# Optimization experiments

Measured on AMD Instinct MI355X. Metric: run time of the kernel, lower is better.

## Reference

```python
import jax, jax.numpy as jnp
import numpy as np

N_NODES = 100000
D = 256
N_TYPES = 4
E1 = 300000
E2 = 300000


def setup_inputs() -> dict:
    key = jax.random.key(0)
    ks = jax.random.split(key, 9)
    x = jax.random.normal(ks[0], (N_NODES, D), dtype=jnp.float32)
    hyperedge_index_s1 = jax.random.randint(ks[1], (2, E1 * 1), 0, N_NODES, dtype=jnp.int32)
    hyperedge_type_s1 = jax.random.randint(ks[2], (E1,), 0, N_TYPES, dtype=jnp.int32)
    hyperedge_index_s2 = jax.random.randint(ks[3], (2, E2 * 2), 0, N_NODES, dtype=jnp.int32)
    hyperedge_type_s2 = jax.random.randint(ks[4], (E2,), 0, N_TYPES, dtype=jnp.int32)
    # xavier_normal init for A: std = sqrt(2 / (fan_in + fan_out))
    A_s1 = jax.random.normal(ks[5], (N_TYPES, 1 * D, D), dtype=jnp.float32) * np.sqrt(2.0 / (D + D)).astype(np.float32)
    A_s2 = jax.random.normal(ks[6], (N_TYPES, 2 * D, D), dtype=jnp.float32) * np.sqrt(2.0 / (2 * D + D)).astype(np.float32)
    lim = 1.0 / np.sqrt(D)
    W_c = jax.random.uniform(ks[7], (D, D), minval=-lim, maxval=lim, dtype=jnp.float32)
    b_c = jax.random.uniform(ks[8], (D,), minval=-lim, maxval=lim, dtype=jnp.float32)
    return dict(x=x,
                hyperedge_index_s1=hyperedge_index_s1, hyperedge_type_s1=hyperedge_type_s1,
                hyperedge_index_s2=hyperedge_index_s2, hyperedge_type_s2=hyperedge_type_s2,
                A_s1=A_s1, A_s2=A_s2, W_c=W_c, b_c=b_c)


def _shape_agg(x, A, idx, etype, shape, n_nodes):
    """Per-hyperedge-shape gather -> per-type matmul -> normalize -> scatter-add."""
    d = x.shape[1]
    e = etype.shape[0]
    # concat the `shape` source node features per hyperedge: [E, shape*d]
    src = x[idx[0]].reshape(e, shape * d)
    # first target slot per hyperedge: [E]
    dst = idx[1].reshape(e, shape)[:, 0]
    agg = jnp.zeros((n_nodes, d), dtype=x.dtype)
    for t in range(A.shape[0]):  # small fixed number of edge types
        mask = etype == t
        tmp = src @ A[t]  # [E, d]
        # per-destination count within this (shape, type) group == torch.unique counts
        counts = jax.ops.segment_sum(mask.astype(x.dtype), dst, num_segments=n_nodes)
        norm = jnp.where(mask, 1.0 / jnp.maximum(counts[dst], 1.0), 0.0)
        agg = agg.at[dst].add(norm[:, None] * tmp)
    return agg


def reference(x, hyperedge_index_s1, hyperedge_type_s1,
              hyperedge_index_s2, hyperedge_type_s2,
              A_s1, A_s2, W_c, b_c):
    n = x.shape[0]
    agg = _shape_agg(x, A_s1, hyperedge_index_s1, hyperedge_type_s1, 1, n)
    agg = agg + _shape_agg(x, A_s2, hyperedge_index_s2, hyperedge_type_s2, 2, n)
    return x @ W_c.T + b_c + agg
```

## Files before the change

### kernel.cpp

```cpp
#include <hip/hip_runtime.h>
#include <stdint.h>

#define N_NODES 100000
#define D 256
#define NT 4

typedef float f32x4 __attribute__((ext_vector_type(4)));
typedef __bf16 bf16x8 __attribute__((ext_vector_type(8)));

__device__ __forceinline__ unsigned short f2bf(float f) {
    unsigned u = __float_as_uint(f);
    u += 0x7FFF + ((u >> 16) & 1);
    return (unsigned short)(u >> 16);
}

__device__ __forceinline__ void gload_lds16(const void* g, void* lds) {
    __builtin_amdgcn_global_load_lds(
        (const __attribute__((address_space(1))) unsigned int*)g,
        (__attribute__((address_space(3))) unsigned int*)lds, 16, 0, 0);
}


template<int SHAPE>
__global__ void k_count(const int* __restrict__ idx, const int* __restrict__ etype,
                        int E, int* __restrict__ counts) {
    int e = blockIdx.x * 256 + threadIdx.x;
    if (e >= E) return;
    int t = etype[e];
    int dst = idx[(size_t)SHAPE * E + (size_t)SHAPE * e];
    atomicAdd(&counts[t * N_NODES + dst], 1);
}


__global__ __launch_bounds__(256) void k_scan1(const int* __restrict__ in, int n,
        int* __restrict__ outv, int* __restrict__ bsums) {
    __shared__ int s[256];
    int tid = threadIdx.x;
    int i = blockIdx.x * 1024 + tid * 4;
    int v0 = 0, v1 = 0, v2 = 0, v3 = 0;
    if (i + 3 < n) {
        int4 v = *(const int4*)(in + i);
        v0 = v.x; v1 = v.y; v2 = v.z; v3 = v.w;
    } else {
        if (i     < n) v0 = in[i];
        if (i + 1 < n) v1 = in[i + 1];
        if (i + 2 < n) v2 = in[i + 2];
        if (i + 3 < n) v3 = in[i + 3];
    }
    int tsum = v0 + v1 + v2 + v3;
    s[tid] = tsum; __syncthreads();
    for (int off = 1; off < 256; off <<= 1) {
        int t = (tid >= off) ? s[tid - off] : 0;
        __syncthreads();
        s[tid] += t;
        __syncthreads();
    }
    int excl = s[tid] - tsum;
    if (tid == 255) bsums[blockIdx.x] = s[255];
    int o0 = excl, o1 = o0 + v0, o2 = o1 + v1, o3 = o2 + v2;
    if (i + 3 < n) {
        *(int4*)(outv + i) = make_int4(o0, o1, o2, o3);
    } else {
        if (i     < n) outv[i]     = o0;
        if (i + 1 < n) outv[i + 1] = o1;
        if (i + 2 < n) outv[i + 2] = o2;
        if (i + 3 < n) outv[i + 3] = o3;
    }
}

__global__ void k_scan2(int* __restrict__ bsums, int nb) {
    __shared__ int s[512];
    int t = threadIdx.x;
    int v = (t < nb) ? bsums[t] : 0;
    s[t] = v; __syncthreads();
    for (int off = 1; off < 512; off <<= 1) {
        int u = (t >= off) ? s[t - off] : 0;
        __syncthreads();
        s[t] += u;
        __syncthreads();
    }
    if (t < nb) bsums[t] = s[t] - v;
}

__global__ __launch_bounds__(256) void k_scan3(int* __restrict__ cellofs,
        int* __restrict__ cellcur, const int* __restrict__ bsums, int n) {
    int i = blockIdx.x * 1024 + threadIdx.x * 4;
    int add = bsums[blockIdx.x];
    if (i + 3 < n) {
        int4 v = *(int4*)(cellofs + i);
        v.x += add; v.y += add; v.z += add; v.w += add;
        *(int4*)(cellofs + i) = v;
        *(int4*)(cellcur + i) = v;
    } else {
        for (int k = 0; k < 4; ++k)
            if (i + k < n) { int v = cellofs[i + k] + add; cellofs[i + k] = v; cellcur[i + k] = v; }
    }
}


template<int SHAPE>
__global__ void k_place(const int* __restrict__ idx, const int* __restrict__ etype, int E,
                        int* __restrict__ cellcur, int* __restrict__ bucket) {
    int e = blockIdx.x * 256 + threadIdx.x;
    if (e >= E) return;
    int t = etype[e];
    int dst = idx[(size_t)SHAPE * E + (size_t)SHAPE * e];
    int pos = atomicAdd(&cellcur[t * N_NODES + dst], 1);
    bucket[pos] = e;
}


__global__ __launch_bounds__(256) void k_cvt(const float* __restrict__ in,
        unsigned short* __restrict__ ob, int n8) {
    int i = blockIdx.x * 256 + threadIdx.x;
    if (i >= n8) return;
    const float4* p = (const float4*)in + (size_t)i * 2;
    float4 v0 = p[0], v1 = p[1];
    union { unsigned short us[8]; uint4 u4; } o;
    o.us[0] = f2bf(v0.x); o.us[1] = f2bf(v0.y); o.us[2] = f2bf(v0.z); o.us[3] = f2bf(v0.w);
    o.us[4] = f2bf(v1.x); o.us[5] = f2bf(v1.y); o.us[6] = f2bf(v1.z); o.us[7] = f2bf(v1.w);
    *(uint4*)(ob + (size_t)i * 8) = o.u4;
}


__global__ void k_cvt_At(const float* __restrict__ A, unsigned short* __restrict__ AT, int K) {
    __shared__ float tl[32][33];
    const float* Ab = A + (size_t)blockIdx.z * K * D;
    unsigned short* Ob = AT + (size_t)blockIdx.z * D * K;
    int k0 = blockIdx.x * 32, j0 = blockIdx.y * 32;
    int lx = threadIdx.x, ly = threadIdx.y;
    for (int yy = ly; yy < 32; yy += 8)
        tl[yy][lx] = Ab[(size_t)(k0 + yy) * D + j0 + lx];
    __syncthreads();
    for (int yy = ly; yy < 32; yy += 8)
        Ob[(size_t)(j0 + yy) * K + k0 + lx] = f2bf(tl[lx][yy]);
}


__global__ __launch_bounds__(256) void k_init_mfma(const unsigned short* __restrict__ xb,
        const unsigned short* __restrict__ Wb, const float* __restrict__ bias,
        float* __restrict__ out, int n) {
    __shared__ __align__(16) char xs[64 * 128];
    int row0 = blockIdx.x * 64;
    int tid = threadIdx.x;
    int lane = tid & 63, w = tid >> 6;
    int l15 = lane & 15, l4 = lane >> 4;
    f32x4 acc[4][4];
    #pragma unroll
    for (int m = 0; m < 4; ++m)
        #pragma unroll
        for (int nn = 0; nn < 4; ++nn) acc[m][nn] = (f32x4)0.f;

    for (int kk = 0; kk < D; kk += 64) {
        #pragma unroll
        for (int it = 0; it < 2; ++it) {
            int f = it * 256 + tid;
            int r = f >> 3, q0 = f & 7;
            int q = q0 ^ (r & 7);
            int gr = row0 + r; if (gr >= n) gr = n - 1;
            gload_lds16(xb + (size_t)gr * D + kk + q * 8, xs + f * 16);
        }
        bf16x8 bfr[2][4];
        #pragma unroll
        for (int ks = 0; ks < 2; ++ks)
            #pragma unroll
            for (int nn = 0; nn < 4; ++nn) {
                int j = w * 64 + nn * 16 + l15;
                int k = kk + ks * 32 + l4 * 8;
                bfr[ks][nn] = *(const bf16x8*)(Wb + (size_t)j * D + k);
            }
        __syncthreads();
        #pragma unroll
        for (int ks = 0; ks < 2; ++ks)
            #pragma unroll
            for (int m = 0; m < 4; ++m) {
                int R = m * 16 + l15;
                int C = ks * 4 + l4;
                bf16x8 a = *(const bf16x8*)(xs + R * 128 + ((C ^ (R & 7)) << 4));
                #pragma unroll
                for (int nn = 0; nn < 4; ++nn)
                    acc[m][nn] = __builtin_amdgcn_mfma_f32_16x16x32_bf16(
                        a, bfr[ks][nn], acc[m][nn], 0, 0, 0);
            }
        __syncthreads();
    }
    #pragma unroll
    for (int m = 0; m < 4; ++m)
        #pragma unroll
        for (int nn = 0; nn < 4; ++nn) {
            int col = w * 64 + nn * 16 + l15;
            float bv = bias[col];
            #pragma unroll
            for (int r = 0; r < 4; ++r) {
                int row = row0 + m * 16 + l4 * 4 + r;
                if (row < n) out[(size_t)row * D + col] = acc[m][nn][r] + bv;
            }
        }
}


template<int SHAPE>
__global__ __launch_bounds__(256) void k_edge_mfma(const unsigned short* __restrict__ xb,
        const int* __restrict__ idx, const unsigned short* __restrict__ AT,
        float* __restrict__ out, int E,
        const int* __restrict__ counts, const int* __restrict__ cellofs,
        const int* __restrict__ bucket) {
    constexpr int K = SHAPE * 256;
    __shared__ __align__(16) char xs[64 * 128];
    __shared__ int srcS[SHAPE][64];
    __shared__ int dstS[64];
    __shared__ float normS[64];

    int t = blockIdx.y;
    int offs_t = cellofs[t * N_NODES];
    int end_t = (t == NT - 1) ? E : cellofs[(t + 1) * N_NODES];
    int cnt = end_t - offs_t;
    int tile = blockIdx.x * 64;
    if (tile >= cnt) return;
    int nE = min(64, cnt - tile);
    int base = offs_t + tile;
    int tid = threadIdx.x;

    if (tid < 64) {
        bool valid = tid < nE;
        int e = bucket[base + (valid ? tid : 0)];
        int dst = idx[(size_t)SHAPE * E + (size_t)SHAPE * e];
        dstS[tid] = dst;
        int c = counts[t * N_NODES + dst];
        normS[tid] = valid ? 1.0f / (float)(c > 1 ? c : 1) : 0.0f;
        srcS[0][tid] = idx[SHAPE * e];
        if (SHAPE == 2) srcS[SHAPE - 1][tid] = idx[SHAPE * e + SHAPE - 1];
    }
    __syncthreads();

    const unsigned short* Bt = AT + (size_t)t * D * K;
    int lane = tid & 63, w = tid >> 6;
    int l15 = lane & 15, l4 = lane >> 4;
    f32x4 acc[4][4];
    #pragma unroll
    for (int m = 0; m < 4; ++m)
        #pragma unroll
        for (int nn = 0; nn < 4; ++nn) acc[m][nn] = (f32x4)0.f;

    for (int kk = 0; kk < K; kk += 64) {
        #pragma unroll
        for (int it = 0; it < 2; ++it) {
            int f = it * 256 + tid;
            int r = f >> 3, q0 = f & 7;
            int q = q0 ^ (r & 7);
            int node = srcS[SHAPE == 2 ? (kk >> 8) : 0][r];
            int col = (kk & 255) + q * 8;
            gload_lds16(xb + (size_t)node * D + col, xs + f * 16);
        }
        bf16x8 bfr[2][4];
        #pragma unroll
        for (int ks = 0; ks < 2; ++ks)
            #pragma unroll
            for (int nn = 0; nn < 4; ++nn) {
                int j = w * 64 + nn * 16 + l15;
                int k = kk + ks * 32 + l4 * 8;
                bfr[ks][nn] = *(const bf16x8*)(Bt + (size_t)j * K + k);
            }
        __syncthreads();
        #pragma unroll
        for (int ks = 0; ks < 2; ++ks)
            #pragma unroll
            for (int m = 0; m < 4; ++m) {
                int R = m * 16 + l15;
                int C = ks * 4 + l4;
                bf16x8 a = *(const bf16x8*)(xs + R * 128 + ((C ^ (R & 7)) << 4));
                #pragma unroll
                for (int nn = 0; nn < 4; ++nn)
                    acc[m][nn] = __builtin_amdgcn_mfma_f32_16x16x32_bf16(
                        a, bfr[ks][nn], acc[m][nn], 0, 0, 0);
            }
        __syncthreads();
    }
    #pragma unroll
    for (int m = 0; m < 4; ++m)
        #pragma unroll
        for (int r = 0; r < 4; ++r) {
            int rr = m * 16 + l4 * 4 + r;
            if (rr < nE) {
                float nm = normS[rr];
                size_t ob = (size_t)dstS[rr] * D;
                #pragma unroll
                for (int nn = 0; nn < 4; ++nn) {
                    int col = w * 64 + nn * 16 + l15;
                    atomicAdd(&out[ob + col], nm * acc[m][nn][r]);
                }
            }
        }
}


extern "C" void kernel_launch(void* const* d_in, const int* in_sizes, int n_in,
                              void* d_out, int out_size, void* d_ws, size_t ws_size,
                              hipStream_t stream) {
    const float* x  = (const float*)d_in[0];
    const int* idx1 = (const int*)d_in[1];
    const int* ty1  = (const int*)d_in[2];
    const int* idx2 = (const int*)d_in[3];
    const int* ty2  = (const int*)d_in[4];
    const float* A1 = (const float*)d_in[5];
    const float* A2 = (const float*)d_in[6];
    const float* W  = (const float*)d_in[7];
    const float* b  = (const float*)d_in[8];
    float* out = (float*)d_out;

    int E1 = in_sizes[2];
    int E2 = in_sizes[4];
    int maxE = E1 > E2 ? E1 : E2;
    const int NCELL = NT * N_NODES;
    const int NB = (NCELL + 1023) / 1024;

    char* p = (char*)d_ws;
    unsigned short* xb  = (unsigned short*)p; p += (size_t)N_NODES * D * 2;
    unsigned short* Wb  = (unsigned short*)p; p += (size_t)D * D * 2;
    unsigned short* A1T = (unsigned short*)p; p += (size_t)NT * D * 256 * 2;
    unsigned short* A2T = (unsigned short*)p; p += (size_t)NT * D * 512 * 2;
    int* counts  = (int*)p; p += (size_t)NCELL * 4;
    int* cellofs = (int*)p; p += (size_t)NCELL * 4;
    int* cellcur = (int*)p; p += (size_t)NCELL * 4;
    int* bsums   = (int*)p; p += 512 * 4;
    int* bucket  = (int*)p; p += (size_t)maxE * 4;

    k_cvt<<<(N_NODES * D / 8 + 255) / 256, 256, 0, stream>>>(x, xb, N_NODES * D / 8);
    k_cvt<<<(D * D / 8 + 255) / 256, 256, 0, stream>>>(W, Wb, D * D / 8);
    k_cvt_At<<<dim3(256 / 32, D / 32, NT), dim3(32, 8), 0, stream>>>(A1, A1T, 256);
    k_cvt_At<<<dim3(512 / 32, D / 32, NT), dim3(32, 8), 0, stream>>>(A2, A2T, 512);

    k_init_mfma<<<(N_NODES + 63) / 64, 256, 0, stream>>>(xb, Wb, b, out, N_NODES);

    hipMemsetAsync(counts, 0, (size_t)NCELL * sizeof(int), stream);
    k_count<1><<<(E1 + 255) / 256, 256, 0, stream>>>(idx1, ty1, E1, counts);
    k_scan1<<<NB, 256, 0, stream>>>(counts, NCELL, cellofs, bsums);
    k_scan2<<<1, 512, 0, stream>>>(bsums, NB);
    k_scan3<<<NB, 256, 0, stream>>>(cellofs, cellcur, bsums, NCELL);
    k_place<1><<<(E1 + 255) / 256, 256, 0, stream>>>(idx1, ty1, E1, cellcur, bucket);
    k_edge_mfma<1><<<dim3((E1 + 63) / 64, NT), 256, 0, stream>>>(
        xb, idx1, A1T, out, E1, counts, cellofs, bucket);

    hipMemsetAsync(counts, 0, (size_t)NCELL * sizeof(int), stream);
    k_count<2><<<(E2 + 255) / 256, 256, 0, stream>>>(idx2, ty2, E2, counts);
    k_scan1<<<NB, 256, 0, stream>>>(counts, NCELL, cellofs, bsums);
    k_scan2<<<1, 512, 0, stream>>>(bsums, NB);
    k_scan3<<<NB, 256, 0, stream>>>(cellofs, cellcur, bsums, NCELL);
    k_place<2><<<(E2 + 255) / 256, 256, 0, stream>>>(idx2, ty2, E2, cellcur, bucket);
    k_edge_mfma<2><<<dim3((E2 + 63) / 64, NT), 256, 0, stream>>>(
        xb, idx2, A2T, out, E2, counts, cellofs, bucket);
}
```

Baseline: 696.6 us.

## Replace per-edge atomic scatter with bf16 scratch buffer and per-node segmented reduce

When workspace allows, the edge MFMA kernel writes normalized per-edge results as bf16 rows into a scratch buffer ordered by (type, destination) bucket instead of doing float atomicAdds into the output. A new reduce kernel then walks each destination's contiguous segments across the four types and adds the sum to the output with one plain read-modify-write. The aim is to remove heavy fp32 atomic traffic. The cost is an extra ~150MB of scratch write plus read per shape, a bf16 rounding of the per-edge contributions, and a larger LDS footprint in the edge kernel.

```diff
diff --git a/kernel.cpp b/kernel.cpp
--- a/kernel.cpp
+++ b/kernel.cpp
@@ -199,10 +199,10 @@
 }
 
 
-template<int SHAPE>
+template<int SHAPE, int SCR>
 __global__ __launch_bounds__(256) void k_edge_mfma(const unsigned short* __restrict__ xb,
         const int* __restrict__ idx, const unsigned short* __restrict__ AT,
-        float* __restrict__ out, int E,
+        float* __restrict__ out, unsigned short* __restrict__ eo, int E,
         const int* __restrict__ counts, const int* __restrict__ cellofs,
         const int* __restrict__ bucket) {
     constexpr int K = SHAPE * 256;
@@ -276,21 +276,79 @@
             }
         __syncthreads();
     }
-    #pragma unroll
-    for (int m = 0; m < 4; ++m)
-        #pragma unroll
-        for (int r = 0; r < 4; ++r) {
-            int rr = m * 16 + l4 * 4 + r;
-            if (rr < nE) {
+
+    if constexpr (SCR) {
+        __shared__ unsigned short re[64][264];
+        #pragma unroll
+        for (int m = 0; m < 4; ++m)
+            #pragma unroll
+            for (int r = 0; r < 4; ++r) {
+                int rr = m * 16 + l4 * 4 + r;
                 float nm = normS[rr];
-                size_t ob = (size_t)dstS[rr] * D;
                 #pragma unroll
                 for (int nn = 0; nn < 4; ++nn) {
                     int col = w * 64 + nn * 16 + l15;
-                    atomicAdd(&out[ob + col], nm * acc[m][nn][r]);
+                    re[rr][col] = f2bf(nm * acc[m][nn][r]);
                 }
             }
+        __syncthreads();
+        #pragma unroll
+        for (int it = 0; it < 8; ++it) {
+            int f = it * 256 + tid;
+            int row = f >> 5, seg = f & 31;
+            if (row < nE) {
+                uint4 v = *(const uint4*)&re[row][seg * 8];
+                *(uint4*)(eo + (size_t)(base + row) * D + seg * 8) = v;
+            }
         }
+    } else {
+        #pragma unroll
+        for (int m = 0; m < 4; ++m)
+            #pragma unroll
+            for (int r = 0; r < 4; ++r) {
+                int rr = m * 16 + l4 * 4 + r;
+                if (rr < nE) {
+                    float nm = normS[rr];
+                    size_t ob = (size_t)dstS[rr] * D;
+                    #pragma unroll
+                    for (int nn = 0; nn < 4; ++nn) {
+                        int col = w * 64 + nn * 16 + l15;
+                        atomicAdd(&out[ob + col], nm * acc[m][nn][r]);
+                    }
+                }
+            }
+    }
+}
+
+
+__global__ __launch_bounds__(256) void k_reduce(const unsigned short* __restrict__ eo,
+        const int* __restrict__ counts, const int* __restrict__ cellofs,
+        float* __restrict__ out) {
+    int wv = threadIdx.x >> 6, lane = threadIdx.x & 63;
+    int dst = blockIdx.x * 4 + wv;
+    if (dst >= N_NODES) return;
+    float a0 = 0.f, a1 = 0.f, a2 = 0.f, a3 = 0.f;
+    int tot = 0;
+    #pragma unroll
+    for (int t = 0; t < NT; ++t) {
+        int start = cellofs[t * N_NODES + dst];
+        int c = counts[t * N_NODES + dst];
+        tot += c;
+        for (int i = 0; i < c; ++i) {
+            const unsigned short* row = eo + (size_t)(start + i) * D + lane * 4;
+            uint2 v = *(const uint2*)row;
+            a0 += __uint_as_float(v.x << 16);
+            a1 += __uint_as_float(v.x & 0xFFFF0000u);
+            a2 += __uint_as_float(v.y << 16);
+            a3 += __uint_as_float(v.y & 0xFFFF0000u);
+        }
+    }
+    if (tot) {
+        float4* o = (float4*)&out[(size_t)dst * D + lane * 4];
+        float4 cur = *o;
+        cur.x += a0; cur.y += a1; cur.z += a2; cur.w += a3;
+        *o = cur;
+    }
 }
 
 
@@ -313,6 +371,7 @@
     int maxE = E1 > E2 ? E1 : E2;
     const int NCELL = NT * N_NODES;
     const int NB = (NCELL + 1023) / 1024;
+    const int NRB = (N_NODES + 3) / 4;
 
     char* p = (char*)d_ws;
     unsigned short* xb  = (unsigned short*)p; p += (size_t)N_NODES * D * 2;
@@ -324,6 +383,8 @@
     int* cellcur = (int*)p; p += (size_t)NCELL * 4;
     int* bsums   = (int*)p; p += 512 * 4;
     int* bucket  = (int*)p; p += (size_t)maxE * 4;
+    unsigned short* eo = (unsigned short*)p; p += (size_t)maxE * D * 2;
+    bool scr = ((size_t)(p - (char*)d_ws)) <= ws_size;
 
     k_cvt<<<(N_NODES * D / 8 + 255) / 256, 256, 0, stream>>>(x, xb, N_NODES * D / 8);
     k_cvt<<<(D * D / 8 + 255) / 256, 256, 0, stream>>>(W, Wb, D * D / 8);
@@ -338,8 +399,14 @@
     k_scan2<<<1, 512, 0, stream>>>(bsums, NB);
     k_scan3<<<NB, 256, 0, stream>>>(cellofs, cellcur, bsums, NCELL);
     k_place<1><<<(E1 + 255) / 256, 256, 0, stream>>>(idx1, ty1, E1, cellcur, bucket);
-    k_edge_mfma<1><<<dim3((E1 + 63) / 64, NT), 256, 0, stream>>>(
-        xb, idx1, A1T, out, E1, counts, cellofs, bucket);
+    if (scr) {
+        k_edge_mfma<1, 1><<<dim3((E1 + 63) / 64, NT), 256, 0, stream>>>(
+            xb, idx1, A1T, out, eo, E1, counts, cellofs, bucket);
+        k_reduce<<<NRB, 256, 0, stream>>>(eo, counts, cellofs, out);
+    } else {
+        k_edge_mfma<1, 0><<<dim3((E1 + 63) / 64, NT), 256, 0, stream>>>(
+            xb, idx1, A1T, out, nullptr, E1, counts, cellofs, bucket);
+    }
 
     hipMemsetAsync(counts, 0, (size_t)NCELL * sizeof(int), stream);
     k_count<2><<<(E2 + 255) / 256, 256, 0, stream>>>(idx2, ty2, E2, counts);
@@ -347,6 +414,12 @@
     k_scan2<<<1, 512, 0, stream>>>(bsums, NB);
     k_scan3<<<NB, 256, 0, stream>>>(cellofs, cellcur, bsums, NCELL);
     k_place<2><<<(E2 + 255) / 256, 256, 0, stream>>>(idx2, ty2, E2, cellcur, bucket);
-    k_edge_mfma<2><<<dim3((E2 + 63) / 64, NT), 256, 0, stream>>>(
-        xb, idx2, A2T, out, E2, counts, cellofs, bucket);
-}
+    if (scr) {
+        k_edge_mfma<2, 1><<<dim3((E2 + 63) / 64, NT), 256, 0, stream>>>(
+            xb, idx2, A2T, out, eo, E2, counts, cellofs, bucket);
+        k_reduce<<<NRB, 256, 0, stream>>>(eo, counts, cellofs, out);
+    } else {
+        k_edge_mfma<2, 0><<<dim3((E2 + 63) / 64, NT), 256, 0, stream>>>(
+            xb, idx2, A2T, out, nullptr, E2, counts, cellofs, bucket);
+    }
+}
```

Result: faster. 640.2 us (-8.1%).
